# Performance work log

Measured on AMD Instinct MI355X. Metric: run time of the kernel, lower is better.

The kernel has to match this reference:

```python
import jax, jax.numpy as jnp
import numpy as np

B, N, DIM, HEADS = 4, 1024, 1024, 16
DH = DIM // HEADS
SCALE = 1.0 / np.sqrt(DH)
EPS = 1e-6


def clinear(x, Wr, Wi, br, bi):
    # (a+bi)(Wr+Wi i): real = a Wr^T - b Wi^T, imag = a Wi^T + b Wr^T
    xr, xi = x.real, x.imag
    real = xr @ Wr.T - xi @ Wi.T + br
    imag = xr @ Wi.T + xi @ Wr.T + bi
    return jax.lax.complex(real, imag)


def cln(x, gamma, beta):
    # normalize magnitude over last dim, keep phase
    mag = jnp.abs(x)
    phase = jnp.angle(x)
    mean = jnp.mean(mag, axis=-1, keepdims=True)
    var = jnp.var(mag, axis=-1, keepdims=True)
    nm = (mag - mean) / jnp.sqrt(var + EPS)
    nm = nm * gamma + beta
    return jax.lax.complex(nm * jnp.cos(phase), nm * jnp.sin(phase))


def forward(xr, xi, Wq_r, Wq_i, bq_r, bq_i, Wk_r, Wk_i, bk_r, bk_i,
            Wv_r, Wv_i, bv_r, bv_i, Wo_r, Wo_i, bo_r, bo_i,
            gq, beq, gk, bek, gv, bev):
    x = jax.lax.complex(xr, xi)  # [B,N,D] complex64

    def heads(t):
        return t.reshape(B, N, HEADS, DH).transpose(0, 2, 1, 3)  # [B,H,N,dh]

    Q = heads(cln(clinear(x, Wq_r, Wq_i, bq_r, bq_i), gq, beq))
    K = heads(cln(clinear(x, Wk_r, Wk_i, bk_r, bk_i), gk, bek))
    V = heads(cln(clinear(x, Wv_r, Wv_i, bv_r, bv_i), gv, bev))

    Qf = jnp.fft.fft(Q, axis=2, norm='ortho')
    Kf = jnp.fft.fft(K, axis=2, norm='ortho')
    Vf = jnp.fft.fft(V, axis=2, norm='ortho')

    scores = jnp.einsum('bhnd,bhmd->bhnm', Qf, jnp.conj(Kf)) * SCALE
    attn = jax.nn.softmax(scores.real, axis=-1)  # real-valued softmax
    # attn is real; multiply into complex Vf componentwise
    out_f = jax.lax.complex(jnp.einsum('bhnm,bhmd->bhnd', attn, Vf.real),
                            jnp.einsum('bhnm,bhmd->bhnd', attn, Vf.imag))
    out = jnp.fft.ifft(out_f, axis=2, norm='ortho')
    out = out.transpose(0, 2, 1, 3).reshape(B, N, DIM)
    y = clinear(out, Wo_r, Wo_i, bo_r, bo_i)
    # return real||imag concatenated on last axis (float32 view of complex output)
    return jnp.concatenate([y.real, y.imag], axis=-1)


def setup_inputs() -> dict:
    key = jax.random.key(0)
    ks = jax.random.split(key, 16)
    wscale = np.sqrt(2.0 / (DIM + DIM)).astype(np.float32)
    d = {}
    d['xr'] = jax.random.normal(ks[0], (B, N, DIM), jnp.float32)
    d['xi'] = jax.random.normal(ks[1], (B, N, DIM), jnp.float32)
    i = 2
    for name in ('q', 'k', 'v', 'o'):
        d[f'W{name}_r'] = jax.random.normal(ks[i], (DIM, DIM), jnp.float32) * wscale; i += 1
        d[f'W{name}_i'] = jax.random.normal(ks[i], (DIM, DIM), jnp.float32) * wscale; i += 1
        d[f'b{name}_r'] = jnp.zeros((DIM,), jnp.float32)
        d[f'b{name}_i'] = jnp.zeros((DIM,), jnp.float32)
    for name in ('q', 'k', 'v'):
        d[f'g{name}'] = jnp.ones((DIM,), jnp.float32)
        d[f'be{name}'] = jnp.zeros((DIM,), jnp.float32)
    return d


def reference(xr, xi, Wq_r, Wq_i, bq_r, bq_i, Wk_r, Wk_i, bk_r, bk_i,
              Wv_r, Wv_i, bv_r, bv_i, Wo_r, Wo_i, bo_r, bo_i,
              gq, beq, gk, bek, gv, bev):
    return forward(xr, xi, Wq_r, Wq_i, bq_r, bq_i, Wk_r, Wk_i, bk_r, bk_i,
                   Wv_r, Wv_i, bv_r, bv_i, Wo_r, Wo_i, bo_r, bo_i,
                   gq, beq, gk, bek, gv, bev)
```

## Files before the change

### kernel.cpp

```cpp
#include <hip/hip_runtime.h>
#include <math.h>

#define BB 4
#define NN 1024
#define DIMM 1024
#define HHH 16
#define DHH 64
#define BN 4096
#define EPS_LN 1e-6f

typedef __bf16 bf16_t;
typedef __bf16 bf16x8 __attribute__((ext_vector_type(8)));
typedef float f32x4 __attribute__((ext_vector_type(4)));
typedef float f32x16 __attribute__((ext_vector_type(16)));
#define MFMA16(a, b, c) __builtin_amdgcn_mfma_f32_16x16x32_bf16(a, b, c, 0, 0, 0)
#define MFMA32(a, b, c) __builtin_amdgcn_mfma_f32_32x32x16_bf16(a, b, c, 0, 0, 0)
#define AS1 __attribute__((address_space(1)))
#define AS3 __attribute__((address_space(3)))

__device__ inline unsigned pk2(float a, float b) {
  union { bf16_t h[2]; unsigned u; } c;
  c.h[0] = (bf16_t)a; c.h[1] = (bf16_t)b;
  return c.u;
}
union U16 { uint4 u; bf16x8 v; };

__global__ __launch_bounds__(256) void pack_x(
    const float* __restrict__ xr, const float* __restrict__ xi,
    bf16_t* __restrict__ out)
{
  int t = blockIdx.x * 256 + threadIdx.x;
  size_t e = (size_t)t * 8;
  int row = (int)(e >> 11), col = (int)(e & 2047);
  const float* src = (col < 1024) ? (xr + (size_t)row * 1024 + col)
                                  : (xi + (size_t)row * 1024 + col - 1024);
  float4 a = *(const float4*)src;
  float4 b = *(const float4*)(src + 4);
  bf16x8 o;
  o[0] = (bf16_t)a.x; o[1] = (bf16_t)a.y; o[2] = (bf16_t)a.z; o[3] = (bf16_t)a.w;
  o[4] = (bf16_t)b.x; o[5] = (bf16_t)b.y; o[6] = (bf16_t)b.z; o[7] = (bf16_t)b.w;
  *(bf16x8*)(out + e) = o;
}

__global__ __launch_bounds__(256) void pack_w(
    const float* __restrict__ Wr, const float* __restrict__ Wi,
    const float* __restrict__ br, const float* __restrict__ bi,
    bf16_t* __restrict__ Wcat, float* __restrict__ bcat)
{
  int t = blockIdx.x * 256 + threadIdx.x;
  size_t e = (size_t)t * 8;
  int row = (int)(e >> 11), col = (int)(e & 2047);
  const float* src;
  float sgn = 1.f;
  if (row < 1024) {
    if (col < 1024) src = Wr + (size_t)row * 1024 + col;
    else          { src = Wi + (size_t)row * 1024 + col - 1024; sgn = -1.f; }
  } else {
    int r2 = row - 1024;
    if (col < 1024) src = Wi + (size_t)r2 * 1024 + col;
    else            src = Wr + (size_t)r2 * 1024 + col - 1024;
  }
  float4 a = *(const float4*)src;
  float4 b = *(const float4*)(src + 4);
  bf16x8 o;
  o[0] = (bf16_t)(sgn * a.x); o[1] = (bf16_t)(sgn * a.y);
  o[2] = (bf16_t)(sgn * a.z); o[3] = (bf16_t)(sgn * a.w);
  o[4] = (bf16_t)(sgn * b.x); o[5] = (bf16_t)(sgn * b.y);
  o[6] = (bf16_t)(sgn * b.z); o[7] = (bf16_t)(sgn * b.w);
  *(bf16x8*)(Wcat + e) = o;
  if (e < 2048) {
#pragma unroll
    for (int j = 0; j < 8; ++j) {
      int n = (int)e + j;
      bcat[n] = (n < 1024) ? br[n] : bi[n - 1024];
    }
  }
}

__global__ __launch_bounds__(256) void gemm_bf16(
    const bf16_t* __restrict__ A, const bf16_t* __restrict__ Bt,
    const float* __restrict__ bias,
    float* __restrict__ Cr, float* __restrict__ Ci, int ldc)
{
  __shared__ bf16_t sA[128 * 64];
  __shared__ bf16_t sB[128 * 64];
  const int tid = threadIdx.x;
  const int w = tid >> 6, l = tid & 63;
  const int lo4 = l & 15, hi = l >> 4;
  const int wr = w >> 1, wc = w & 1;
  const int row0 = blockIdx.y * 128, col0 = blockIdx.x * 128;

  const int srow = (l >> 3);
  const int scol = (l & 7) * 8;
  const bf16_t* gA[4];
  const bf16_t* gB[4];
#pragma unroll
  for (int i = 0; i < 4; ++i) {
    int r = (w * 4 + i) * 8 + srow;
    gA[i] = A  + (size_t)(row0 + r) * 2048 + scol;
    gB[i] = Bt + (size_t)(col0 + r) * 2048 + scol;
  }

  f32x4 acc[4][4] = {};
  for (int k0 = 0; k0 < 2048; k0 += 64) {
    __syncthreads();
#pragma unroll
    for (int i = 0; i < 4; ++i) {
      __builtin_amdgcn_global_load_lds((const AS1 void*)(gA[i] + k0),
                                       (AS3 void*)&sA[(w * 4 + i) * 512], 16, 0, 0);
      __builtin_amdgcn_global_load_lds((const AS1 void*)(gB[i] + k0),
                                       (AS3 void*)&sB[(w * 4 + i) * 512], 16, 0, 0);
    }
    __syncthreads();
#pragma unroll
    for (int kk = 0; kk < 2; ++kk) {
      bf16x8 am[4], bn[4];
#pragma unroll
      for (int i = 0; i < 4; ++i)
        am[i] = *(const bf16x8*)&sA[(wr * 64 + i * 16 + lo4) * 64 + kk * 32 + hi * 8];
#pragma unroll
      for (int j = 0; j < 4; ++j)
        bn[j] = *(const bf16x8*)&sB[(wc * 64 + j * 16 + lo4) * 64 + kk * 32 + hi * 8];
#pragma unroll
      for (int i = 0; i < 4; ++i)
#pragma unroll
        for (int j = 0; j < 4; ++j)
          acc[i][j] = MFMA16(am[i], bn[j], acc[i][j]);
    }
  }
  const int colg0 = col0 + wc * 64;
  float* Cp = (colg0 < 1024) ? Cr : Ci;
  const int cb = colg0 & 1023;
#pragma unroll
  for (int i = 0; i < 4; ++i) {
#pragma unroll
    for (int j = 0; j < 4; ++j) {
      float bv = bias[colg0 + j * 16 + lo4];
#pragma unroll
      for (int r = 0; r < 4; ++r) {
        int rowg = row0 + wr * 64 + i * 16 + hi * 4 + r;
        Cp[(size_t)rowg * ldc + cb + j * 16 + lo4] = acc[i][j][r] + bv;
      }
    }
  }
}

__global__ __launch_bounds__(256) void ln_stats(
    const float* __restrict__ re, const float* __restrict__ im,
    float2* __restrict__ st)
{
  __shared__ float red[8];
  const int row = blockIdx.x;
  const int tid = threadIdx.x;
  const float* pr = re + (size_t)row * DIMM;
  const float* pi = im + (size_t)row * DIMM;
  float s = 0.f, s2 = 0.f;
#pragma unroll
  for (int t = 0; t < 4; ++t) {
    int c = tid + t * 256;
    float vr = pr[c], vi = pi[c];
    float mg = sqrtf(vr * vr + vi * vi);
    s += mg; s2 += mg * mg;
  }
#pragma unroll
  for (int o = 32; o; o >>= 1) { s += __shfl_down(s, o); s2 += __shfl_down(s2, o); }
  if ((tid & 63) == 0) { red[tid >> 6] = s; red[4 + (tid >> 6)] = s2; }
  __syncthreads();
  if (tid == 0) {
    float S = red[0] + red[1] + red[2] + red[3];
    float S2 = red[4] + red[5] + red[6] + red[7];
    float mean = S * (1.f / DIMM);
    float var = S2 * (1.f / DIMM) - mean * mean;
    st[row] = make_float2(mean, rsqrtf(var + EPS_LN));
  }
}

#define LIDX(d_, c_) (((d_) << 10) + ((c_) ^ (((c_) >> 5) & 31) ^ (((d_) & 7) << 2)))

__global__ __launch_bounds__(512) void fft_kernel(
    const float* __restrict__ inR, const float* __restrict__ inI,
    bf16_t* __restrict__ outR, bf16_t* __restrict__ outI,
    int in_sb, int in_sh, int in_sn, int in_sd,
    int out_sb, int out_sh, int out_sn,
    float sign, float oscale, int imode, int omode,
    const float2* __restrict__ stats,
    const float* __restrict__ gamma, const float* __restrict__ beta)
{
  __shared__ float lr[8 * 1024], li[8 * 1024];
  __shared__ float2 tw[1024];
  const int tid = threadIdx.x;
  const int dc = blockIdx.x & 7;
  const int bh = blockIdx.x >> 3;
  const int b = bh >> 4, h = bh & 15;
  const float* bR = inR + (size_t)b * in_sb + (size_t)h * in_sh;
  const float* bI = inI + (size_t)b * in_sb + (size_t)h * in_sh;
#pragma unroll
  for (int t = tid; t < 1024; t += 512) {
    float ang = sign * 3.14159265358979323846f * (float)t * (1.f / 512.f);
    float sn, cs;
    __sincosf(ang, &sn, &cs);
    tw[t] = make_float2(cs, sn);
  }
  if (imode == 0) {
    float gg[8], bb[8];
    if (stats) {
#pragma unroll
      for (int ds = 0; ds < 8; ++ds) {
        gg[ds] = gamma[h * DHH + dc * 8 + ds];
        bb[ds] = beta[h * DHH + dc * 8 + ds];
      }
    }
#pragma unroll
    for (int rep = 0; rep < 2; ++rep) {
      int n = tid + rep * 512;
      const float* pR = bR + (size_t)n * in_sn + dc * 8;
      const float* pI = bI + (size_t)n * in_sn + dc * 8;
      union { float4 q[2]; float f[8]; } ur, ui;
      ur.q[0] = *(const float4*)pR;      ur.q[1] = *(const float4*)(pR + 4);
      ui.q[0] = *(const float4*)pI;      ui.q[1] = *(const float4*)(pI + 4);
      if (stats) {
        float2 stv = stats[b * NN + n];
#pragma unroll
        for (int ds = 0; ds < 8; ++ds) {
          float a = ur.f[ds], c2 = ui.f[ds];
          float mag = sqrtf(a * a + c2 * c2);
          float nm = (mag - stv.x) * stv.y * gg[ds] + bb[ds];
          if (mag > 0.f) { float sc = nm / mag; ur.f[ds] = a * sc; ui.f[ds] = c2 * sc; }
          else           { ur.f[ds] = nm; ui.f[ds] = 0.f; }
        }
      }
#pragma unroll
      for (int ds = 0; ds < 8; ++ds) {
        int ax = LIDX(ds, n);
        lr[ax] = ur.f[ds];
        li[ax] = ui.f[ds];
      }
    }
  } else {
    const int ds = tid & 7, nb = tid >> 3;
    const float* pR = bR + (size_t)(dc * 8 + ds) * in_sd + nb * 16;
    const float* pI = bI + (size_t)(dc * 8 + ds) * in_sd + nb * 16;
#pragma unroll
    for (int k = 0; k < 16; k += 4) {
      float4 v = *(const float4*)(pR + k);
      float4 w = *(const float4*)(pI + k);
      int c = nb * 16 + k;
      lr[LIDX(ds, c + 0)] = v.x;  li[LIDX(ds, c + 0)] = w.x;
      lr[LIDX(ds, c + 1)] = v.y;  li[LIDX(ds, c + 1)] = w.y;
      lr[LIDX(ds, c + 2)] = v.z;  li[LIDX(ds, c + 2)] = w.z;
      lr[LIDX(ds, c + 3)] = v.w;  li[LIDX(ds, c + 3)] = w.w;
    }
  }
  __syncthreads();
  const int dsub = tid & 7;
  const int jb = tid >> 3;
  int lq2 = 8;
  for (int st = 0; st < 5; ++st) {
    const int qtr = 1 << lq2;
    const int tmul = 1 << (2 * st);
    for (int jt = 0; jt < 4; ++jt) {
      int j = jb + jt * 64;
      int o = j & (qtr - 1);
      int i0 = ((j >> lq2) << (lq2 + 2)) + o;
      int a0 = LIDX(dsub, i0);
      int a1 = LIDX(dsub, i0 + qtr);
      int a2 = LIDX(dsub, i0 + 2 * qtr);
      int a3 = LIDX(dsub, i0 + 3 * qtr);
      float x0r = lr[a0], x0i = li[a0];
      float x1r = lr[a1], x1i = li[a1];
      float x2r = lr[a2], x2i = li[a2];
      float x3r = lr[a3], x3i = li[a3];
      float ar = x0r + x2r, ai2 = x0i + x2i;
      float br = x0r - x2r, bi  = x0i - x2i;
      float cr = x1r + x3r, ci  = x1i + x3i;
      float dr = x1r - x3r, di  = x1i - x3i;
      float2 t1 = tw[o * tmul];
      float2 t2 = tw[2 * o * tmul];
      float2 t3 = tw[3 * o * tmul];
      lr[a0] = ar + cr;  li[a0] = ai2 + ci;
      float u1r = br - sign * di, u1i = bi + sign * dr;
      lr[a1] = u1r * t1.x - u1i * t1.y;  li[a1] = u1r * t1.y + u1i * t1.x;
      float u2r = ar - cr, u2i = ai2 - ci;
      lr[a2] = u2r * t2.x - u2i * t2.y;  li[a2] = u2r * t2.y + u2i * t2.x;
      float u3r = br + sign * di, u3i = bi - sign * dr;
      lr[a3] = u3r * t3.x - u3i * t3.y;  li[a3] = u3r * t3.y + u3i * t3.x;
    }
    __syncthreads();
    lq2 -= 2;
  }
  bf16_t* oRb = outR + (size_t)b * out_sb + (size_t)h * out_sh;
  bf16_t* oIb = outI + (size_t)b * out_sb + (size_t)h * out_sh;
#pragma unroll
  for (int rep = 0; rep < 2; ++rep) {
    int n = tid + rep * 512;
    int rv2 = __brev((unsigned)n) >> 22;
    int p = ((rv2 & 0x155) << 1) | ((rv2 >> 1) & 0x155);
    float fr[8], fi[8];
#pragma unroll
    for (int ds = 0; ds < 8; ++ds) {
      fr[ds] = lr[LIDX(ds, p)] * oscale;
      fi[ds] = li[LIDX(ds, p)] * oscale;
    }
    if (omode == 1) {
      size_t tb = (size_t)(n >> 5) * 4096;
#pragma unroll
      for (int ds = 0; ds < 8; ++ds) {
        int dch = dc * 8 + ds;
        size_t ga = tb + (size_t)dch * 32 + ((n & 31) ^ (((dch >> 1) & 3) << 3));
        oRb[ga] = (bf16_t)fr[ds];
        oIb[ga] = (bf16_t)fi[ds];
      }
    } else {
      int cb = dc * 8;
      if (omode == 2) cb = (dc ^ (n & 7)) * 8;
      bf16x8 v0, w0;
#pragma unroll
      for (int k = 0; k < 8; ++k) {
        v0[k] = (bf16_t)fr[k];
        w0[k] = (bf16_t)fi[k];
      }
      size_t gb = (size_t)n * out_sn + cb;
      *(bf16x8*)(oRb + gb) = v0;
      *(bf16x8*)(oIb + gb) = w0;
    }
  }
}

__global__ __launch_bounds__(256, 2) void fattn(
    const bf16_t* __restrict__ Qf, const bf16_t* __restrict__ Kfs,
    const bf16_t* __restrict__ Vfs, float* __restrict__ OT)
{
  __shared__ bf16_t K2[2][4096];
  __shared__ bf16_t V2[2][4096];
  const int tid = threadIdx.x;
  const int w = tid >> 6, l = tid & 63;
  const int lq = l & 31;
  const int h = l >> 5;
  const int i = blockIdx.x;
  const int j = i >> 3;
  const int bh = (i & 7) * 8 + (j >> 3);
  const int q0 = (j & 7) * 128 + w * 32;

  bf16x8 bq[8];
  const bf16_t* qp = Qf + ((size_t)bh * NN + q0 + lq) * 128 + h * 8;
#pragma unroll
  for (int kk = 0; kk < 8; ++kk) bq[kk] = *(const bf16x8*)(qp + kk * 16);

  f32x16 o[4] = {};
  float m = -3e38f, ln = 0.f;

  const bf16_t* kg = Kfs + (size_t)bh * 131072 + w * 1024 + l * 8;
  const bf16_t* vg = Vfs + (size_t)bh * 131072 + w * 1024 + l * 8;
  const int kswz = (lq & 7) << 3;
  const int vswz = ((lq >> 1) & 3) << 3;

#pragma unroll
  for (int ii = 0; ii < 2; ++ii) {
    __builtin_amdgcn_global_load_lds((const AS1 void*)(kg + ii * 512),
                                     (AS3 void*)&K2[0][w * 1024 + ii * 512], 16, 0, 0);
    __builtin_amdgcn_global_load_lds((const AS1 void*)(vg + ii * 512),
                                     (AS3 void*)&V2[0][w * 1024 + ii * 512], 16, 0, 0);
  }
  __syncthreads();

  int cur = 0;
  for (int t = 0; t < 32; ++t) {
    if (t < 31) {
      const bf16_t* kt = kg + (size_t)(t + 1) * 4096;
      const bf16_t* vt = vg + (size_t)(t + 1) * 4096;
#pragma unroll
      for (int ii = 0; ii < 2; ++ii) {
        __builtin_amdgcn_global_load_lds((const AS1 void*)(kt + ii * 512),
                                         (AS3 void*)&K2[cur ^ 1][w * 1024 + ii * 512], 16, 0, 0);
        __builtin_amdgcn_global_load_lds((const AS1 void*)(vt + ii * 512),
                                         (AS3 void*)&V2[cur ^ 1][w * 1024 + ii * 512], 16, 0, 0);
      }
    }

    f32x16 s = {};
#pragma unroll
    for (int kk = 0; kk < 8; ++kk) {
      bf16x8 ak = *(const bf16x8*)&K2[cur][lq * 128 + ((kk * 16 + h * 8) ^ kswz)];
      s = MFMA32(ak, bq[kk], s);
    }

    float pmax = s[0];
#pragma unroll
    for (int r = 1; r < 16; ++r) pmax = fmaxf(pmax, s[r]);
    pmax = fmaxf(pmax, __shfl_xor(pmax, 32));
    if (!__all(pmax - m <= 8.f)) {
      float mnew = fmaxf(m, pmax);
      float alpha = __expf(m - mnew);
      m = mnew;
      ln *= alpha;
#pragma unroll
      for (int db = 0; db < 4; ++db)
#pragma unroll
        for (int r = 0; r < 16; ++r) o[db][r] *= alpha;
    }
    float pf[16];
    float rs = 0.f;
#pragma unroll
    for (int r = 0; r < 16; ++r) { pf[r] = __expf(s[r] - m); rs += pf[r]; }
    rs += __shfl_xor(rs, 32);
    ln += rs;

    unsigned pw[8];
#pragma unroll
    for (int ii = 0; ii < 8; ++ii) pw[ii] = pk2(pf[2 * ii], pf[2 * ii + 1]);
    unsigned r0 = (unsigned)__shfl_xor((int)(h ? pw[0] : pw[2]), 32);
    unsigned r1 = (unsigned)__shfl_xor((int)(h ? pw[1] : pw[3]), 32);
    unsigned r2 = (unsigned)__shfl_xor((int)(h ? pw[4] : pw[6]), 32);
    unsigned r3 = (unsigned)__shfl_xor((int)(h ? pw[5] : pw[7]), 32);
    U16 bp0, bp1;
    bp0.u.x = h ? r0 : pw[0];  bp0.u.y = h ? r1 : pw[1];
    bp0.u.z = h ? pw[2] : r0;  bp0.u.w = h ? pw[3] : r1;
    bp1.u.x = h ? r2 : pw[4];  bp1.u.y = h ? r3 : pw[5];
    bp1.u.z = h ? pw[6] : r2;  bp1.u.w = h ? pw[7] : r3;

#pragma unroll
    for (int db = 0; db < 4; ++db) {
      int r = db * 32 + lq;
      bf16x8 av0 = *(const bf16x8*)&V2[cur][r * 32 + ((h * 8) ^ vswz)];
      bf16x8 av1 = *(const bf16x8*)&V2[cur][r * 32 + ((16 + h * 8) ^ vswz)];
      o[db] = MFMA32(av0, bp0.v, o[db]);
      o[db] = MFMA32(av1, bp1.v, o[db]);
    }

    __syncthreads();
    cur ^= 1;
  }

  float inv = 1.f / ln;
  const size_t otb = (size_t)bh * 128 * NN + q0 + lq;
#pragma unroll
  for (int db = 0; db < 4; ++db)
#pragma unroll
    for (int r = 0; r < 16; ++r) {
      int dl = (r & 3) + 8 * (r >> 2) + 4 * h;
      OT[otb + (size_t)(db * 32 + dl) * NN] = o[db][r] * inv;
    }
}

extern "C" void kernel_launch(void* const* d_in, const int* in_sizes, int n_in,
                              void* d_out, int out_size, void* d_ws, size_t ws_size,
                              hipStream_t stream) {
  const float* xr   = (const float*)d_in[0];
  const float* xi   = (const float*)d_in[1];
  const float* Wqr  = (const float*)d_in[2];
  const float* Wqi  = (const float*)d_in[3];
  const float* bqr  = (const float*)d_in[4];
  const float* bqi  = (const float*)d_in[5];
  const float* Wkr  = (const float*)d_in[6];
  const float* Wki  = (const float*)d_in[7];
  const float* bkr  = (const float*)d_in[8];
  const float* bki  = (const float*)d_in[9];
  const float* Wvr  = (const float*)d_in[10];
  const float* Wvi  = (const float*)d_in[11];
  const float* bvr  = (const float*)d_in[12];
  const float* bvi  = (const float*)d_in[13];
  const float* Wor  = (const float*)d_in[14];
  const float* Woi  = (const float*)d_in[15];
  const float* bor  = (const float*)d_in[16];
  const float* boi  = (const float*)d_in[17];
  const float* gq   = (const float*)d_in[18];
  const float* beq  = (const float*)d_in[19];
  const float* gk   = (const float*)d_in[20];
  const float* bek  = (const float*)d_in[21];
  const float* gv   = (const float*)d_in[22];
  const float* bev  = (const float*)d_in[23];

  char* wp = (char*)d_ws;
  bf16_t* Axaug = (bf16_t*)wp;  wp += (size_t)4096 * 2048 * 2;
  bf16_t* Wcat  = (bf16_t*)wp;  wp += (size_t)2048 * 2048 * 2;
  float*  bcat  = (float*)wp;   wp += (size_t)2048 * 4;
  float2* lnst  = (float2*)wp;  wp += (size_t)4096 * 8;
  float*  Ar    = (float*)wp;   wp += (size_t)4096 * 1024 * 4;
  float*  Ai    = (float*)wp;   wp += (size_t)4096 * 1024 * 4;
  bf16_t* Qf    = (bf16_t*)wp;  wp += (size_t)64 * 1024 * 128 * 2;
  bf16_t* Kf    = (bf16_t*)wp;  wp += (size_t)64 * 1024 * 128 * 2;
  bf16_t* VfT   = (bf16_t*)wp;  wp += (size_t)64 * 1024 * 128 * 2;
  bf16_t* Yaug  = Qf;
  float*  OT    = Ar;

  const dim3 gGemm(16, 32);
  const int gPackX = (4096 * 2048 / 8) / 256;
  const int gPackW = (2048 * 2048 / 8) / 256;
  const int gFft = 64 * 8;
  const int gAtt = 64 * 8;

  pack_x<<<gPackX, 256, 0, stream>>>(xr, xi, Axaug);

  pack_w<<<gPackW, 256, 0, stream>>>(Wqr, Wqi, bqr, bqi, Wcat, bcat);
  gemm_bf16<<<gGemm, 256, 0, stream>>>(Axaug, Wcat, bcat, Ar, Ai, 1024);
  ln_stats<<<BN, 256, 0, stream>>>(Ar, Ai, lnst);
  fft_kernel<<<gFft, 512, 0, stream>>>(Ar, Ai, Qf, Qf + 64,
      NN * DIMM, DHH, DIMM, 1,
      16 * NN * 128, NN * 128, 128,
      -1.0f, 0.03125f * 0.125f, 0, 0, lnst, gq, beq);
  pack_w<<<gPackW, 256, 0, stream>>>(Wkr, Wki, bkr, bki, Wcat, bcat);
  gemm_bf16<<<gGemm, 256, 0, stream>>>(Axaug, Wcat, bcat, Ar, Ai, 1024);
  ln_stats<<<BN, 256, 0, stream>>>(Ar, Ai, lnst);
  fft_kernel<<<gFft, 512, 0, stream>>>(Ar, Ai, Kf, Kf + 64,
      NN * DIMM, DHH, DIMM, 1,
      16 * NN * 128, NN * 128, 128,
      -1.0f, 0.03125f, 0, 2, lnst, gk, bek);
  pack_w<<<gPackW, 256, 0, stream>>>(Wvr, Wvi, bvr, bvi, Wcat, bcat);
  gemm_bf16<<<gGemm, 256, 0, stream>>>(Axaug, Wcat, bcat, Ar, Ai, 1024);
  ln_stats<<<BN, 256, 0, stream>>>(Ar, Ai, lnst);
  fft_kernel<<<gFft, 512, 0, stream>>>(Ar, Ai, VfT, VfT + 2048,
      NN * DIMM, DHH, DIMM, 1,
      16 * 131072, 131072, 0,
      -1.0f, 0.03125f, 0, 1, lnst, gv, bev);
  fattn<<<gAtt, 256, 0, stream>>>(Qf, Kf, VfT, OT);
  fft_kernel<<<gFft, 512, 0, stream>>>(OT, OT + (size_t)64 * NN, Yaug, Yaug + 1024,
      16 * 128 * NN, 128 * NN, 1, NN,
      NN * 2048, 64, 2048,
      +1.0f, 0.03125f, 1, 0, nullptr, nullptr, nullptr);
  float* yout = (float*)d_out;
  pack_w<<<gPackW, 256, 0, stream>>>(Wor, Woi, bor, boi, Wcat, bcat);
  gemm_bf16<<<gGemm, 256, 0, stream>>>(Yaug, Wcat, bcat, yout, yout + 1024, 2048);
}
```

Baseline: 431.7 us.

## Triple-buffer K/V tiles in frequency attention with partial vmcnt waits

```diff
diff --git a/kernel.cpp b/kernel.cpp
--- a/kernel.cpp
+++ b/kernel.cpp
@@ -330,8 +330,8 @@
     const bf16_t* __restrict__ Qf, const bf16_t* __restrict__ Kfs,
     const bf16_t* __restrict__ Vfs, float* __restrict__ OT)
 {
-  __shared__ bf16_t K2[2][4096];
-  __shared__ bf16_t V2[2][4096];
+  __shared__ bf16_t K3[3][4096];
+  __shared__ bf16_t V3[3][4096];
   const int tid = threadIdx.x;
   const int w = tid >> 6, l = tid & 63;
   const int lq = l & 31;
@@ -355,32 +355,40 @@
   const int vswz = ((lq >> 1) & 3) << 3;
 
 #pragma unroll
-  for (int ii = 0; ii < 2; ++ii) {
-    __builtin_amdgcn_global_load_lds((const AS1 void*)(kg + ii * 512),
-                                     (AS3 void*)&K2[0][w * 1024 + ii * 512], 16, 0, 0);
-    __builtin_amdgcn_global_load_lds((const AS1 void*)(vg + ii * 512),
-                                     (AS3 void*)&V2[0][w * 1024 + ii * 512], 16, 0, 0);
-  }
-  __syncthreads();
+  for (int tt = 0; tt < 2; ++tt) {
+    const bf16_t* kt = kg + (size_t)tt * 4096;
+    const bf16_t* vt = vg + (size_t)tt * 4096;
+#pragma unroll
+    for (int ii = 0; ii < 2; ++ii) {
+      __builtin_amdgcn_global_load_lds((const AS1 void*)(kt + ii * 512),
+                                       (AS3 void*)&K3[tt][w * 1024 + ii * 512], 16, 0, 0);
+      __builtin_amdgcn_global_load_lds((const AS1 void*)(vt + ii * 512),
+                                       (AS3 void*)&V3[tt][w * 1024 + ii * 512], 16, 0, 0);
+    }
+  }
+  asm volatile("s_waitcnt vmcnt(4)" ::: "memory");
+  __builtin_amdgcn_s_barrier();
+  __builtin_amdgcn_sched_barrier(0);
 
   int cur = 0;
   for (int t = 0; t < 32; ++t) {
-    if (t < 31) {
-      const bf16_t* kt = kg + (size_t)(t + 1) * 4096;
-      const bf16_t* vt = vg + (size_t)(t + 1) * 4096;
+    if (t < 30) {
+      int nb = cur + 2; if (nb >= 3) nb -= 3;
+      const bf16_t* kt = kg + (size_t)(t + 2) * 4096;
+      const bf16_t* vt = vg + (size_t)(t + 2) * 4096;
 #pragma unroll
       for (int ii = 0; ii < 2; ++ii) {
         __builtin_amdgcn_global_load_lds((const AS1 void*)(kt + ii * 512),
-                                         (AS3 void*)&K2[cur ^ 1][w * 1024 + ii * 512], 16, 0, 0);
+                                         (AS3 void*)&K3[nb][w * 1024 + ii * 512], 16, 0, 0);
         __builtin_amdgcn_global_load_lds((const AS1 void*)(vt + ii * 512),
-                                         (AS3 void*)&V2[cur ^ 1][w * 1024 + ii * 512], 16, 0, 0);
+                                         (AS3 void*)&V3[nb][w * 1024 + ii * 512], 16, 0, 0);
       }
     }
 
     f32x16 s = {};
 #pragma unroll
     for (int kk = 0; kk < 8; ++kk) {
-      bf16x8 ak = *(const bf16x8*)&K2[cur][lq * 128 + ((kk * 16 + h * 8) ^ kswz)];
+      bf16x8 ak = *(const bf16x8*)&K3[cur][lq * 128 + ((kk * 16 + h * 8) ^ kswz)];
       s = MFMA32(ak, bq[kk], s);
     }
 
@@ -421,14 +429,19 @@
 #pragma unroll
     for (int db = 0; db < 4; ++db) {
       int r = db * 32 + lq;
-      bf16x8 av0 = *(const bf16x8*)&V2[cur][r * 32 + ((h * 8) ^ vswz)];
-      bf16x8 av1 = *(const bf16x8*)&V2[cur][r * 32 + ((16 + h * 8) ^ vswz)];
+      bf16x8 av0 = *(const bf16x8*)&V3[cur][r * 32 + ((h * 8) ^ vswz)];
+      bf16x8 av1 = *(const bf16x8*)&V3[cur][r * 32 + ((16 + h * 8) ^ vswz)];
       o[db] = MFMA32(av0, bp0.v, o[db]);
       o[db] = MFMA32(av1, bp1.v, o[db]);
     }
 
-    __syncthreads();
-    cur ^= 1;
+    if (t < 31) {
+      if (t < 30) asm volatile("s_waitcnt vmcnt(4)" ::: "memory");
+      else        asm volatile("s_waitcnt vmcnt(0)" ::: "memory");
+      __builtin_amdgcn_s_barrier();
+      __builtin_amdgcn_sched_barrier(0);
+    }
+    cur = (cur == 2) ? 0 : cur + 1;
   }
 
   float inv = 1.f / ln;
```

Result: no change. 431.4 us (-0.1%).
